# Performance work log

Hardware: AMD Instinct MI355X
Metric: run time of the kernel (lower is better)

## Reference

```python
import jax, jax.numpy as jnp
import numpy as np

X = Y = 512   # x_width = y_width
B = 8         # batch (<= bsize)
C = 32        # hidden_dim / num_feats
N_WARP = 3    # warp hidden layers
N_REND = 3    # renderer hidden layers
LRELU = 0.001


def _layer_norm(x, g, b, eps=1e-5):
    mu = x.mean(-1, keepdims=True)
    var = ((x - mu) ** 2).mean(-1, keepdims=True)
    return (x - mu) * jax.lax.rsqrt(var + eps) * g + b


def _grid_sample(img, grid):
    # img: (C,H,W) shared across batch; grid: (B,Hg,Wg,2) in [-1,1] (x,y)
    # bilinear, padding_mode='zeros', align_corners=False (torch defaults)
    Cc, H, W = img.shape
    ix = ((grid[..., 0] + 1.0) * W - 1.0) * 0.5
    iy = ((grid[..., 1] + 1.0) * H - 1.0) * 0.5
    x0f = jnp.floor(ix)
    y0f = jnp.floor(iy)
    wx1 = ix - x0f
    wy1 = iy - y0f

    def gather(xf, yf):
        valid = (xf >= 0) & (xf <= W - 1) & (yf >= 0) & (yf <= H - 1)
        xi = jnp.clip(xf, 0, W - 1).astype(jnp.int32)
        yi = jnp.clip(yf, 0, H - 1).astype(jnp.int32)
        v = img[:, yi, xi]                     # (C,B,Hg,Wg)
        return jnp.where(valid[None], v, 0.0)

    g00 = gather(x0f, y0f)
    g01 = gather(x0f + 1, y0f)
    g10 = gather(x0f, y0f + 1)
    g11 = gather(x0f + 1, y0f + 1)
    out = (g00 * ((1 - wx1) * (1 - wy1))[None]
           + g01 * (wx1 * (1 - wy1))[None]
           + g10 * ((1 - wx1) * wy1)[None]
           + g11 * (wx1 * wy1)[None])          # (C,B,Hg,Wg)
    return out.transpose(1, 0, 2, 3)           # (B,C,Hg,Wg)


def setup_inputs() -> dict:
    key = jax.random.key(0)
    ks = jax.random.split(key, 10)
    t = jax.random.uniform(ks[0], (B,), minval=-0.5, maxval=0.5)
    data = 0.1 * jax.random.normal(ks[1], (X, Y, C), dtype=jnp.float32)

    # G_FeatureTensor precomputed bilinear indices/weights (ds_factor=1)
    half = 0.5 / X
    xs = np.linspace(half, 1 - half, X, dtype=np.float64)
    xv, yv = np.meshgrid(xs, xs, indexing='ij')
    xy = np.stack([yv.ravel(), xv.ravel()], 1)          # (N,2) col0=yv col1=xv
    s = xy * np.array([X, Y], dtype=np.float64)
    idx = s.astype(np.int64)
    lerp_w = jnp.asarray(s - idx, dtype=jnp.float32)    # (N,2)
    x0 = jnp.asarray(np.clip(idx[:, 0], 0, X - 1), dtype=jnp.int32)
    y0 = jnp.asarray(np.clip(idx[:, 1], 0, Y - 1), dtype=jnp.int32)
    x1 = jnp.minimum(x0 + 1, X - 1)
    y1 = jnp.minimum(y0 + 1, Y - 1)

    lin = np.linspace(-1, 1, X, dtype=np.float32)
    gx, gy = np.meshgrid(lin, lin, indexing='xy')
    xy_basis = jnp.asarray(np.stack([gx, gy], -1))      # (X,Y,2)

    def lw(k, fan_in, shape):
        return (1.0 / np.sqrt(fan_in)) * jax.random.normal(k, shape, dtype=jnp.float32)

    kw = jax.random.split(ks[2], 8)
    return {
        't': t, 'data': data, 'lerp_w': lerp_w, 'xy_basis': xy_basis,
        'w_in': lw(kw[0], 3, (3, C)), 'b_in': jnp.zeros((C,)),
        'w_h': lw(kw[1], C, (N_WARP, C, C)), 'b_h': jnp.zeros((N_WARP, C)),
        'ln_g': jnp.ones((N_WARP, C)), 'ln_b': jnp.zeros((N_WARP, C)),
        'w_out': lw(kw[2], C, (C, 2)), 'b_out': jnp.zeros((2,)),
        'r_wh': lw(kw[3], C, (N_REND, C, C)), 'r_bh': jnp.zeros((N_REND, C)),
        'r_wo': lw(kw[4], C, (C, 1)), 'r_bo': jnp.zeros((1,)),
        'x0': x0, 'y0': y0, 'x1': x1, 'y1': y1,
    }


def reference(t, data, lerp_w, xy_basis, w_in, b_in, w_h, b_h, ln_g, ln_b,
              w_out, b_out, r_wh, r_bh, r_wo, r_bo, x0, y0, x1, y1):
    Bn = t.shape[0]
    wA = lerp_w[:, 0:1]
    wB = lerp_w[:, 1:2]
    # manual 4-corner bilinear gather over the learned feature grid
    feats = (data[y0, x0] * (1 - wA) * (1 - wB)
             + data[y0, x1] * wA * (1 - wB)
             + data[y1, x0] * (1 - wA) * wB
             + data[y1, x1] * wA * wB)                  # (N,C)
    feat_img = feats.reshape(X, Y, C).transpose(2, 0, 1)  # (C,X,Y)

    alpha = (t + 0.5)[:, None]                          # (B,1)
    t_emb = jnp.broadcast_to(alpha[:, None, None, :], (Bn, X, Y, 1))
    t_in = jnp.concatenate(
        [jnp.broadcast_to(xy_basis, (Bn, X, Y, 2)), t_emb], -1)  # (B,X,Y,3)

    h = t_in @ w_in + b_in
    for i in range(N_WARP):
        h = jnp.sin(_layer_norm(h @ w_h[i] + b_h[i], ln_g[i], ln_b[i]))
    motion = (h @ w_out + b_out) * 0.1                  # (B,X,Y,2)

    grid = motion + xy_basis                             # (B,X,Y,2)
    f = _grid_sample(feat_img, grid)                     # (B,C,X,Y)

    z = f.transpose(0, 2, 3, 1)
    for i in range(N_REND):
        z = jax.nn.relu(z @ r_wh[i] + r_bh[i])
    out = (z @ r_wo + r_bo).transpose(0, 3, 1, 2)        # (B,1,X,Y)
    return jnp.where(out >= 0, out, LRELU * out)
```

## Files before the change

### kernel.cpp

```cpp
#include <hip/hip_runtime.h>

#define XDIM 512
#define CDIM 32
#define NPIX (XDIM * XDIM)
#define NB 8

typedef short bf16x8 __attribute__((ext_vector_type(8)));
typedef float f32x4 __attribute__((ext_vector_type(4)));
typedef float f32x16 __attribute__((ext_vector_type(16)));

#define FEATS_BYTES (NPIX * CDIM * 4)

__device__ __forceinline__ short f2bf(float v) {
    __bf16 b = (__bf16)v;
    return __builtin_bit_cast(short, b);
}
__device__ __forceinline__ float bfup(short s) {
    return (float)__builtin_bit_cast(__bf16, s);
}

__global__ __launch_bounds__(64) void wprep_kernel(
    const float* __restrict__ w_h, const float* __restrict__ r_wh,
    unsigned short* __restrict__ afrag)
{
    int L = blockIdx.x >> 1;
    int T = blockIdx.x & 1;
    int l = threadIdx.x;
    const float* W = (L < 3) ? (w_h + L * CDIM * CDIM) : (r_wh + (L - 3) * CDIM * CDIM);
    int m = l & 31;
    int h = l >> 5;
    unsigned short* dh = afrag + (((L * 2 + T) * 2 + 0) * 64 + l) * 8;
    unsigned short* dl = afrag + (((L * 2 + T) * 2 + 1) * 64 + l) * 8;
    for (int j = 0; j < 8; j++) {
        int c = 16 * T + 4 * h + (j & 3) + 8 * (j >> 2);
        float v = W[c * CDIM + m];
        short hi = f2bf(v);
        short lo = f2bf(v - bfup(hi));
        dh[j] = (unsigned short)hi;
        dl[j] = (unsigned short)lo;
    }
}

__global__ __launch_bounds__(256) void feats_kernel(
    const float* __restrict__ data, const float* __restrict__ lerp_w,
    const int* __restrict__ x0, const int* __restrict__ y0,
    const int* __restrict__ x1, const int* __restrict__ y1,
    float* __restrict__ feats)
{
    int tid = blockIdx.x * 256 + threadIdx.x;
    int p = tid >> 5;
    int c = tid & 31;
    if (p >= NPIX) return;
    float wA = lerp_w[p * 2 + 0];
    float wB = lerp_w[p * 2 + 1];
    int xa = x0[p], ya = y0[p], xb = x1[p], yb = y1[p];
    float v00 = data[(ya * XDIM + xa) * CDIM + c];
    float v01 = data[(ya * XDIM + xb) * CDIM + c];
    float v10 = data[(yb * XDIM + xa) * CDIM + c];
    float v11 = data[(yb * XDIM + xb) * CDIM + c];
    float r = v00 * (1.f - wA) * (1.f - wB) + v01 * wA * (1.f - wB)
            + v10 * (1.f - wA) * wB + v11 * wA * wB;
    feats[p * CDIM + c] = r;
}

__device__ __forceinline__ void build2(const float a[16], bf16x8 bh[2], bf16x8 bl[2]) {
    #pragma unroll
    for (int r = 0; r < 16; r++) {
        short hi = f2bf(a[r]);
        bh[r >> 3][r & 7] = hi;
        bl[r >> 3][r & 7] = f2bf(a[r] - bfup(hi));
    }
}

__device__ __forceinline__ void matmul_split(
    const bf16x8 fh[2], const bf16x8 fl[2],
    const bf16x8 bh[2], const bf16x8 bl[2],
    f32x16& accA, f32x16& accB)
{
    f32x16 z = {0.f, 0.f, 0.f, 0.f, 0.f, 0.f, 0.f, 0.f,
                0.f, 0.f, 0.f, 0.f, 0.f, 0.f, 0.f, 0.f};
    accA = z; accB = z;
    accA = __builtin_amdgcn_mfma_f32_32x32x16_bf16(fl[0], bh[0], accA, 0, 0, 0);
    accB = __builtin_amdgcn_mfma_f32_32x32x16_bf16(fl[1], bh[1], accB, 0, 0, 0);
    accA = __builtin_amdgcn_mfma_f32_32x32x16_bf16(fh[0], bl[0], accA, 0, 0, 0);
    accB = __builtin_amdgcn_mfma_f32_32x32x16_bf16(fh[1], bl[1], accB, 0, 0, 0);
    accA = __builtin_amdgcn_mfma_f32_32x32x16_bf16(fh[0], bh[0], accA, 0, 0, 0);
    accB = __builtin_amdgcn_mfma_f32_32x32x16_bf16(fh[1], bh[1], accB, 0, 0, 0);
}

__device__ __forceinline__ void warp_layer(
    float a[16], const bf16x8 fh[2], const bf16x8 fl[2],
    const float* __restrict__ bias, const float* __restrict__ gamma,
    const float* __restrict__ beta, int h)
{
    bf16x8 bh[2], bl[2];
    build2(a, bh, bl);
    f32x16 accA, accB;
    matmul_split(fh, fl, bh, bl, accA, accB);

    float sum = 0.f, sq = 0.f;
    #pragma unroll
    for (int g = 0; g < 4; g++) {
        f32x4 bia = *(const f32x4*)(bias + 8 * g + 4 * h);
        #pragma unroll
        for (int i = 0; i < 4; i++) {
            int r = 4 * g + i;
            float v = (accA[r] + accB[r]) + bia[i];
            a[r] = v;
            sum += v;
            sq = fmaf(v, v, sq);
        }
    }
    sum += __shfl_xor(sum, 32, 64);
    sq  += __shfl_xor(sq, 32, 64);
    float mu = sum * (1.f / 32.f);
    float var = fmaf(sq, 1.f / 32.f, -mu * mu);
    float rs = rsqrtf(var + 1e-5f);
    #pragma unroll
    for (int g = 0; g < 4; g++) {
        f32x4 gg = *(const f32x4*)(gamma + 8 * g + 4 * h);
        f32x4 be = *(const f32x4*)(beta + 8 * g + 4 * h);
        #pragma unroll
        for (int i = 0; i < 4; i++) {
            int r = 4 * g + i;
            a[r] = __sinf(fmaf((a[r] - mu) * rs, gg[i], be[i]));
        }
    }
}

__device__ __forceinline__ void render_layer(
    float a[16], const bf16x8 fh[2], const bf16x8 fl[2],
    const float* __restrict__ bias, int h)
{
    bf16x8 bh[2], bl[2];
    build2(a, bh, bl);
    f32x16 accA, accB;
    matmul_split(fh, fl, bh, bl, accA, accB);
    #pragma unroll
    for (int g = 0; g < 4; g++) {
        f32x4 bia = *(const f32x4*)(bias + 8 * g + 4 * h);
        #pragma unroll
        for (int i = 0; i < 4; i++) {
            int r = 4 * g + i;
            a[r] = fmaxf((accA[r] + accB[r]) + bia[i], 0.f);
        }
    }
}

#define LOADFRAG(L, FH, FL) do { \
    FH[0] = ap[(((L) * 2 + 0) * 2 + 0) * 64 + lane]; \
    FL[0] = ap[(((L) * 2 + 0) * 2 + 1) * 64 + lane]; \
    FH[1] = ap[(((L) * 2 + 1) * 2 + 0) * 64 + lane]; \
    FL[1] = ap[(((L) * 2 + 1) * 2 + 1) * 64 + lane]; \
} while (0)

__global__ __launch_bounds__(256, 4) void fused_mfma_kernel(
    const float* __restrict__ t, const float* __restrict__ xy_basis,
    const float* __restrict__ w_in, const float* __restrict__ b_in,
    const float* __restrict__ b_h,
    const float* __restrict__ ln_g, const float* __restrict__ ln_b,
    const float* __restrict__ w_out, const float* __restrict__ b_out,
    const float* __restrict__ r_bh,
    const float* __restrict__ r_wo, const float* __restrict__ r_bo,
    const float* __restrict__ feats, const unsigned short* __restrict__ afrag,
    float* __restrict__ out)
{
    int lane = threadIdx.x & 63;
    int p = lane & 31, h = lane >> 5;

    int bid = blockIdx.x;
    int swz = (bid & 7) * 2048 + (bid >> 3);
    int gw = swz * 4 + (int)(threadIdx.x >> 6);
    int b = gw & 7;
    int pbase = (gw >> 3) << 5;
    int pix = pbase + p;

    const bf16x8* ap = (const bf16x8*)afrag;

    bf16x8 fAh[2], fAl[2], fBh[2], fBl[2], fCh[2], fCl[2];
    LOADFRAG(0, fAh, fAl);
    LOADFRAG(1, fBh, fBl);

    float alpha = t[b] + 0.5f;
    float2 xy = ((const float2*)xy_basis)[pix];

    float a[16];
    #pragma unroll
    for (int g = 0; g < 4; g++) {
        int c = 8 * g + 4 * h;
        f32x4 w0 = *(const f32x4*)(w_in + c);
        f32x4 w1 = *(const f32x4*)(w_in + CDIM + c);
        f32x4 w2 = *(const f32x4*)(w_in + 2 * CDIM + c);
        f32x4 bb = *(const f32x4*)(b_in + c);
        #pragma unroll
        for (int i = 0; i < 4; i++)
            a[4 * g + i] = fmaf(xy.x, w0[i], fmaf(xy.y, w1[i], fmaf(alpha, w2[i], bb[i])));
    }

    warp_layer(a, fAh, fAl, b_h + 0 * CDIM, ln_g + 0 * CDIM, ln_b + 0 * CDIM, h);
    LOADFRAG(2, fCh, fCl);
    warp_layer(a, fBh, fBl, b_h + 1 * CDIM, ln_g + 1 * CDIM, ln_b + 1 * CDIM, h);
    warp_layer(a, fCh, fCl, b_h + 2 * CDIM, ln_g + 2 * CDIM, ln_b + 2 * CDIM, h);

    float mx = 0.f, my = 0.f;
    #pragma unroll
    for (int g = 0; g < 4; g++) {
        int c = 8 * g + 4 * h;
        f32x4 wa = *(const f32x4*)(w_out + 2 * c);
        f32x4 wb = *(const f32x4*)(w_out + 2 * c + 4);
        mx = fmaf(a[4 * g + 0], wa[0], mx); my = fmaf(a[4 * g + 0], wa[1], my);
        mx = fmaf(a[4 * g + 1], wa[2], mx); my = fmaf(a[4 * g + 1], wa[3], my);
        mx = fmaf(a[4 * g + 2], wb[0], mx); my = fmaf(a[4 * g + 2], wb[1], my);
        mx = fmaf(a[4 * g + 3], wb[2], mx); my = fmaf(a[4 * g + 3], wb[3], my);
    }
    mx += __shfl_xor(mx, 32, 64);
    my += __shfl_xor(my, 32, 64);
    float gridx = fmaf(mx + b_out[0], 0.1f, xy.x);
    float gridy = fmaf(my + b_out[1], 0.1f, xy.y);

    bf16x8 r0h[2], r0l[2], r1h[2], r1l[2], r2h[2], r2l[2];
    LOADFRAG(3, r0h, r0l);
    LOADFRAG(4, r1h, r1l);
    LOADFRAG(5, r2h, r2l);

    float ix = ((gridx + 1.0f) * (float)XDIM - 1.0f) * 0.5f;
    float iy = ((gridy + 1.0f) * (float)XDIM - 1.0f) * 0.5f;
    float x0f = floorf(ix), y0f = floorf(iy);
    float wx = ix - x0f, wy = iy - y0f;
    #pragma unroll
    for (int r = 0; r < 16; r++) a[r] = 0.f;
    #pragma unroll
    for (int corner = 0; corner < 4; corner++) {
        float xf = x0f + (float)(corner & 1);
        float yf = y0f + (float)(corner >> 1);
        float w = ((corner & 1) ? wx : 1.f - wx) * ((corner >> 1) ? wy : 1.f - wy);
        bool valid = (xf >= 0.f) && (xf <= (float)(XDIM - 1)) &&
                     (yf >= 0.f) && (yf <= (float)(XDIM - 1));
        if (!valid) w = 0.f;
        int xi = (int)fminf(fmaxf(xf, 0.f), (float)(XDIM - 1));
        int yi = (int)fminf(fmaxf(yf, 0.f), (float)(XDIM - 1));
        const float* fp = feats + (yi * XDIM + xi) * CDIM + 4 * h;
        #pragma unroll
        for (int g = 0; g < 4; g++) {
            f32x4 v = *(const f32x4*)(fp + 8 * g);
            #pragma unroll
            for (int i = 0; i < 4; i++)
                a[4 * g + i] = fmaf(w, v[i], a[4 * g + i]);
        }
    }

    render_layer(a, r0h, r0l, r_bh + 0 * CDIM, h);
    render_layer(a, r1h, r1l, r_bh + 1 * CDIM, h);
    render_layer(a, r2h, r2l, r_bh + 2 * CDIM, h);

    float o = 0.f;
    #pragma unroll
    for (int g = 0; g < 4; g++) {
        f32x4 wz = *(const f32x4*)(r_wo + 8 * g + 4 * h);
        #pragma unroll
        for (int i = 0; i < 4; i++) o = fmaf(a[4 * g + i], wz[i], o);
    }
    o += __shfl_xor(o, 32, 64);
    o += r_bo[0];
    o = (o >= 0.f) ? o : 0.001f * o;
    if (h == 0) out[b * NPIX + pix] = o;
}

extern "C" void kernel_launch(void* const* d_in, const int* in_sizes, int n_in,
                              void* d_out, int out_size, void* d_ws, size_t ws_size,
                              hipStream_t stream) {
    const float* t        = (const float*)d_in[0];
    const float* data     = (const float*)d_in[1];
    const float* lerp_w   = (const float*)d_in[2];
    const float* xy_basis = (const float*)d_in[3];
    const float* w_in     = (const float*)d_in[4];
    const float* b_in     = (const float*)d_in[5];
    const float* w_h      = (const float*)d_in[6];
    const float* b_h      = (const float*)d_in[7];
    const float* ln_g     = (const float*)d_in[8];
    const float* ln_b     = (const float*)d_in[9];
    const float* w_out    = (const float*)d_in[10];
    const float* b_out    = (const float*)d_in[11];
    const float* r_wh     = (const float*)d_in[12];
    const float* r_bh     = (const float*)d_in[13];
    const float* r_wo     = (const float*)d_in[14];
    const float* r_bo     = (const float*)d_in[15];
    const int* x0 = (const int*)d_in[16];
    const int* y0 = (const int*)d_in[17];
    const int* x1 = (const int*)d_in[18];
    const int* y1 = (const int*)d_in[19];

    float* feats = (float*)d_ws;
    unsigned short* afrag = (unsigned short*)((char*)d_ws + FEATS_BYTES);
    float* out = (float*)d_out;

    wprep_kernel<<<12, 64, 0, stream>>>(w_h, r_wh, afrag);
    feats_kernel<<<(NPIX * CDIM) / 256, 256, 0, stream>>>(data, lerp_w, x0, y0, x1, y1, feats);
    fused_mfma_kernel<<<(NB * NPIX) / 128, 256, 0, stream>>>(
        t, xy_basis, w_in, b_in, b_h, ln_g, ln_b, w_out, b_out,
        r_bh, r_wo, r_bo, feats, afrag, out);
}
```

Baseline: 321.0 us.

## Split fused kernel into separate warp-MLP and render kernels via grid buffer

Splits the single fused per-pixel kernel into two launches: one computes the warp MLP and writes sampling coordinates to a workspace buffer, the other reads them, does the bilinear feature gather and runs the renderer MLP. The aim is lower register pressure and better latency hiding for the gather in each kernel, since each only holds its own weight fragments. The cost is an extra launch and a round trip of 16 MB of grid data through global memory. It falls back to the fused kernel if the workspace is too small.

Result: slower. 328.5 us (+2.3%).

```diff
diff --git a/kernel.cpp b/kernel.cpp
--- a/kernel.cpp
+++ b/kernel.cpp
@@ -10,6 +10,9 @@
 typedef float f32x16 __attribute__((ext_vector_type(16)));
 
 #define FEATS_BYTES (NPIX * CDIM * 4)
+#define AFRAG_BYTES 32768
+#define GRID_BYTES (NB * NPIX * 8)
+#define WS_NEED (FEATS_BYTES + AFRAG_BYTES + GRID_BYTES)
 
 __device__ __forceinline__ short f2bf(float v) {
     __bf16 b = (__bf16)v;
@@ -154,6 +157,131 @@
     FL[1] = ap[(((L) * 2 + 1) * 2 + 1) * 64 + lane]; \
 } while (0)
 
+#define PIXMAP() \
+    int lane = threadIdx.x & 63; \
+    int p = lane & 31, h = lane >> 5; \
+    int bid = blockIdx.x; \
+    int swz = (bid & 7) * 2048 + (bid >> 3); \
+    int gw = swz * 4 + (int)(threadIdx.x >> 6); \
+    int b = gw & 7; \
+    int pbase = (gw >> 3) << 5; \
+    int pix = pbase + p;
+
+__global__ __launch_bounds__(256, 4) void warp_kernel(
+    const float* __restrict__ t, const float* __restrict__ xy_basis,
+    const float* __restrict__ w_in, const float* __restrict__ b_in,
+    const float* __restrict__ b_h,
+    const float* __restrict__ ln_g, const float* __restrict__ ln_b,
+    const float* __restrict__ w_out, const float* __restrict__ b_out,
+    const unsigned short* __restrict__ afrag, float2* __restrict__ grid)
+{
+    PIXMAP();
+    const bf16x8* ap = (const bf16x8*)afrag;
+
+    bf16x8 fAh[2], fAl[2], fBh[2], fBl[2], fCh[2], fCl[2];
+    LOADFRAG(0, fAh, fAl);
+    LOADFRAG(1, fBh, fBl);
+
+    float alpha = t[b] + 0.5f;
+    float2 xy = ((const float2*)xy_basis)[pix];
+
+    float a[16];
+    #pragma unroll
+    for (int g = 0; g < 4; g++) {
+        int c = 8 * g + 4 * h;
+        f32x4 w0 = *(const f32x4*)(w_in + c);
+        f32x4 w1 = *(const f32x4*)(w_in + CDIM + c);
+        f32x4 w2 = *(const f32x4*)(w_in + 2 * CDIM + c);
+        f32x4 bb = *(const f32x4*)(b_in + c);
+        #pragma unroll
+        for (int i = 0; i < 4; i++)
+            a[4 * g + i] = fmaf(xy.x, w0[i], fmaf(xy.y, w1[i], fmaf(alpha, w2[i], bb[i])));
+    }
+
+    warp_layer(a, fAh, fAl, b_h + 0 * CDIM, ln_g + 0 * CDIM, ln_b + 0 * CDIM, h);
+    LOADFRAG(2, fCh, fCl);
+    warp_layer(a, fBh, fBl, b_h + 1 * CDIM, ln_g + 1 * CDIM, ln_b + 1 * CDIM, h);
+    warp_layer(a, fCh, fCl, b_h + 2 * CDIM, ln_g + 2 * CDIM, ln_b + 2 * CDIM, h);
+
+    float mx = 0.f, my = 0.f;
+    #pragma unroll
+    for (int g = 0; g < 4; g++) {
+        int c = 8 * g + 4 * h;
+        f32x4 wa = *(const f32x4*)(w_out + 2 * c);
+        f32x4 wb = *(const f32x4*)(w_out + 2 * c + 4);
+        mx = fmaf(a[4 * g + 0], wa[0], mx); my = fmaf(a[4 * g + 0], wa[1], my);
+        mx = fmaf(a[4 * g + 1], wa[2], mx); my = fmaf(a[4 * g + 1], wa[3], my);
+        mx = fmaf(a[4 * g + 2], wb[0], mx); my = fmaf(a[4 * g + 2], wb[1], my);
+        mx = fmaf(a[4 * g + 3], wb[2], mx); my = fmaf(a[4 * g + 3], wb[3], my);
+    }
+    mx += __shfl_xor(mx, 32, 64);
+    my += __shfl_xor(my, 32, 64);
+    float gridx = fmaf(mx + b_out[0], 0.1f, xy.x);
+    float gridy = fmaf(my + b_out[1], 0.1f, xy.y);
+    if (h == 0) grid[b * NPIX + pix] = make_float2(gridx, gridy);
+}
+
+__global__ __launch_bounds__(256, 4) void render_kernel(
+    const float2* __restrict__ grid,
+    const float* __restrict__ r_bh,
+    const float* __restrict__ r_wo, const float* __restrict__ r_bo,
+    const float* __restrict__ feats, const unsigned short* __restrict__ afrag,
+    float* __restrict__ out)
+{
+    PIXMAP();
+    const bf16x8* ap = (const bf16x8*)afrag;
+
+    bf16x8 r0h[2], r0l[2], r1h[2], r1l[2], r2h[2], r2l[2];
+    LOADFRAG(3, r0h, r0l);
+    LOADFRAG(4, r1h, r1l);
+    LOADFRAG(5, r2h, r2l);
+
+    float2 gxy = grid[b * NPIX + pix];
+
+    float ix = ((gxy.x + 1.0f) * (float)XDIM - 1.0f) * 0.5f;
+    float iy = ((gxy.y + 1.0f) * (float)XDIM - 1.0f) * 0.5f;
+    float x0f = floorf(ix), y0f = floorf(iy);
+    float wx = ix - x0f, wy = iy - y0f;
+    float a[16];
+    #pragma unroll
+    for (int r = 0; r < 16; r++) a[r] = 0.f;
+    #pragma unroll
+    for (int corner = 0; corner < 4; corner++) {
+        float xf = x0f + (float)(corner & 1);
+        float yf = y0f + (float)(corner >> 1);
+        float w = ((corner & 1) ? wx : 1.f - wx) * ((corner >> 1) ? wy : 1.f - wy);
+        bool valid = (xf >= 0.f) && (xf <= (float)(XDIM - 1)) &&
+                     (yf >= 0.f) && (yf <= (float)(XDIM - 1));
+        if (!valid) w = 0.f;
+        int xi = (int)fminf(fmaxf(xf, 0.f), (float)(XDIM - 1));
+        int yi = (int)fminf(fmaxf(yf, 0.f), (float)(XDIM - 1));
+        const float* fp = feats + (yi * XDIM + xi) * CDIM + 4 * h;
+        #pragma unroll
+        for (int g = 0; g < 4; g++) {
+            f32x4 v = *(const f32x4*)(fp + 8 * g);
+            #pragma unroll
+            for (int i = 0; i < 4; i++)
+                a[4 * g + i] = fmaf(w, v[i], a[4 * g + i]);
+        }
+    }
+
+    render_layer(a, r0h, r0l, r_bh + 0 * CDIM, h);
+    render_layer(a, r1h, r1l, r_bh + 1 * CDIM, h);
+    render_layer(a, r2h, r2l, r_bh + 2 * CDIM, h);
+
+    float o = 0.f;
+    #pragma unroll
+    for (int g = 0; g < 4; g++) {
+        f32x4 wz = *(const f32x4*)(r_wo + 8 * g + 4 * h);
+        #pragma unroll
+        for (int i = 0; i < 4; i++) o = fmaf(a[4 * g + i], wz[i], o);
+    }
+    o += __shfl_xor(o, 32, 64);
+    o += r_bo[0];
+    o = (o >= 0.f) ? o : 0.001f * o;
+    if (h == 0) out[b * NPIX + pix] = o;
+}
+
 __global__ __launch_bounds__(256, 4) void fused_mfma_kernel(
     const float* __restrict__ t, const float* __restrict__ xy_basis,
     const float* __restrict__ w_in, const float* __restrict__ b_in,
@@ -165,16 +293,7 @@
     const float* __restrict__ feats, const unsigned short* __restrict__ afrag,
     float* __restrict__ out)
 {
-    int lane = threadIdx.x & 63;
-    int p = lane & 31, h = lane >> 5;
-
-    int bid = blockIdx.x;
-    int swz = (bid & 7) * 2048 + (bid >> 3);
-    int gw = swz * 4 + (int)(threadIdx.x >> 6);
-    int b = gw & 7;
-    int pbase = (gw >> 3) << 5;
-    int pix = pbase + p;
-
+    PIXMAP();
     const bf16x8* ap = (const bf16x8*)afrag;
 
     bf16x8 fAh[2], fAl[2], fBh[2], fBl[2], fCh[2], fCl[2];
@@ -292,11 +411,20 @@
 
     float* feats = (float*)d_ws;
     unsigned short* afrag = (unsigned short*)((char*)d_ws + FEATS_BYTES);
+    float2* grid = (float2*)((char*)d_ws + FEATS_BYTES + AFRAG_BYTES);
     float* out = (float*)d_out;
 
     wprep_kernel<<<12, 64, 0, stream>>>(w_h, r_wh, afrag);
     feats_kernel<<<(NPIX * CDIM) / 256, 256, 0, stream>>>(data, lerp_w, x0, y0, x1, y1, feats);
-    fused_mfma_kernel<<<(NB * NPIX) / 128, 256, 0, stream>>>(
-        t, xy_basis, w_in, b_in, b_h, ln_g, ln_b, w_out, b_out,
-        r_bh, r_wo, r_bo, feats, afrag, out);
-}
+
+    if (ws_size >= (size_t)WS_NEED) {
+        warp_kernel<<<(NB * NPIX) / 128, 256, 0, stream>>>(
+            t, xy_basis, w_in, b_in, b_h, ln_g, ln_b, w_out, b_out, afrag, grid);
+        render_kernel<<<(NB * NPIX) / 128, 256, 0, stream>>>(
+            grid, r_bh, r_wo, r_bo, feats, afrag, out);
+    } else {
+        fused_mfma_kernel<<<(NB * NPIX) / 128, 256, 0, stream>>>(
+            t, xy_basis, w_in, b_in, b_h, ln_g, ln_b, w_out, b_out,
+            r_bh, r_wo, r_bo, feats, afrag, out);
+    }
+}
```

## Fold first renderer layer into feature grid before grid sampling

Applied to the files above, without the earlier changes.

Bilinear grid sampling is linear, so the first renderer matmul is now applied once per grid pixel in a new y_kernel, rather than once per batch item after sampling. The fused kernel samples the pre-multiplied features and then only adds the bias and ReLU for that layer, skipping its MFMA work across all eight batch items. This adds an extra pass over the 32 MB feature buffer, done in place, which is safe only because each pixel's 32 channels sit in one wavefront. It also wraps the MFMA sequence in s_setprio to raise wave priority during matrix ops.

After: 644.1 us. 2.01x slower.

```diff
diff --git a/kernel.cpp b/kernel.cpp
--- a/kernel.cpp
+++ b/kernel.cpp
@@ -63,6 +63,20 @@
     feats[p * CDIM + c] = r;
 }
 
+__global__ __launch_bounds__(256) void y_kernel(
+    const float* __restrict__ r_wh, float* __restrict__ feats)
+{
+    int tid = blockIdx.x * 256 + threadIdx.x;
+    int p = tid >> 5;
+    int c = tid & 31;
+    const float* f = feats + p * CDIM;
+    float acc = 0.f;
+    #pragma unroll
+    for (int k = 0; k < CDIM; k++)
+        acc = fmaf(f[k], r_wh[k * CDIM + c], acc);
+    feats[p * CDIM + c] = acc;
+}
+
 __device__ __forceinline__ void build2(const float a[16], bf16x8 bh[2], bf16x8 bl[2]) {
     #pragma unroll
     for (int r = 0; r < 16; r++) {
@@ -80,12 +94,14 @@
     f32x16 z = {0.f, 0.f, 0.f, 0.f, 0.f, 0.f, 0.f, 0.f,
                 0.f, 0.f, 0.f, 0.f, 0.f, 0.f, 0.f, 0.f};
     accA = z; accB = z;
+    __builtin_amdgcn_s_setprio(1);
     accA = __builtin_amdgcn_mfma_f32_32x32x16_bf16(fl[0], bh[0], accA, 0, 0, 0);
     accB = __builtin_amdgcn_mfma_f32_32x32x16_bf16(fl[1], bh[1], accB, 0, 0, 0);
     accA = __builtin_amdgcn_mfma_f32_32x32x16_bf16(fh[0], bl[0], accA, 0, 0, 0);
     accB = __builtin_amdgcn_mfma_f32_32x32x16_bf16(fh[1], bl[1], accB, 0, 0, 0);
     accA = __builtin_amdgcn_mfma_f32_32x32x16_bf16(fh[0], bh[0], accA, 0, 0, 0);
     accB = __builtin_amdgcn_mfma_f32_32x32x16_bf16(fh[1], bh[1], accB, 0, 0, 0);
+    __builtin_amdgcn_s_setprio(0);
 }
 
 __device__ __forceinline__ void warp_layer(
@@ -162,7 +178,7 @@
     const float* __restrict__ w_out, const float* __restrict__ b_out,
     const float* __restrict__ r_bh,
     const float* __restrict__ r_wo, const float* __restrict__ r_bo,
-    const float* __restrict__ feats, const unsigned short* __restrict__ afrag,
+    const float* __restrict__ yimg, const unsigned short* __restrict__ afrag,
     float* __restrict__ out)
 {
     int lane = threadIdx.x & 63;
@@ -218,8 +234,7 @@
     float gridx = fmaf(mx + b_out[0], 0.1f, xy.x);
     float gridy = fmaf(my + b_out[1], 0.1f, xy.y);
 
-    bf16x8 r0h[2], r0l[2], r1h[2], r1l[2], r2h[2], r2l[2];
-    LOADFRAG(3, r0h, r0l);
+    bf16x8 r1h[2], r1l[2], r2h[2], r2l[2];
     LOADFRAG(4, r1h, r1l);
     LOADFRAG(5, r2h, r2l);
 
@@ -239,7 +254,7 @@
         if (!valid) w = 0.f;
         int xi = (int)fminf(fmaxf(xf, 0.f), (float)(XDIM - 1));
         int yi = (int)fminf(fmaxf(yf, 0.f), (float)(XDIM - 1));
-        const float* fp = feats + (yi * XDIM + xi) * CDIM + 4 * h;
+        const float* fp = yimg + (yi * XDIM + xi) * CDIM + 4 * h;
         #pragma unroll
         for (int g = 0; g < 4; g++) {
             f32x4 v = *(const f32x4*)(fp + 8 * g);
@@ -248,8 +263,14 @@
                 a[4 * g + i] = fmaf(w, v[i], a[4 * g + i]);
         }
     }
-
-    render_layer(a, r0h, r0l, r_bh + 0 * CDIM, h);
+    #pragma unroll
+    for (int g = 0; g < 4; g++) {
+        f32x4 bia = *(const f32x4*)(r_bh + 0 * CDIM + 8 * g + 4 * h);
+        #pragma unroll
+        for (int i = 0; i < 4; i++)
+            a[4 * g + i] = fmaxf(a[4 * g + i] + bia[i], 0.f);
+    }
+
     render_layer(a, r1h, r1l, r_bh + 1 * CDIM, h);
     render_layer(a, r2h, r2l, r_bh + 2 * CDIM, h);
 
@@ -296,6 +317,7 @@
 
     wprep_kernel<<<12, 64, 0, stream>>>(w_h, r_wh, afrag);
     feats_kernel<<<(NPIX * CDIM) / 256, 256, 0, stream>>>(data, lerp_w, x0, y0, x1, y1, feats);
+    y_kernel<<<(NPIX * CDIM) / 256, 256, 0, stream>>>(r_wh, feats);
     fused_mfma_kernel<<<(NB * NPIX) / 128, 256, 0, stream>>>(
         t, xy_basis, w_in, b_in, b_h, ln_g, ln_b, w_out, b_out,
         r_bh, r_wo, r_bo, feats, afrag, out);
```

## Process two batch items per wavefront to reuse weight fragments and add ILP

Applied to the files above, without the earlier changes.

Each wavefront now handles the same 32 pixels for two batch indices (b and b+4), interleaving the warp MLP, gather and render layers for both. Weight fragments and bias loads are shared across the two items, the grid halves, and the independent MFMA chains can overlap. The cost is roughly double the live accumulator registers, and the occupancy hint of 4 blocks per SM was dropped from launch bounds, so occupancy may fall.

New measurement: 270.1 us. -15.9%, faster.

```diff
diff --git a/kernel.cpp b/kernel.cpp
--- a/kernel.cpp
+++ b/kernel.cpp
@@ -147,61 +147,10 @@
     }
 }
 
-#define LOADFRAG(L, FH, FL) do { \
-    FH[0] = ap[(((L) * 2 + 0) * 2 + 0) * 64 + lane]; \
-    FL[0] = ap[(((L) * 2 + 0) * 2 + 1) * 64 + lane]; \
-    FH[1] = ap[(((L) * 2 + 1) * 2 + 0) * 64 + lane]; \
-    FL[1] = ap[(((L) * 2 + 1) * 2 + 1) * 64 + lane]; \
-} while (0)
-
-__global__ __launch_bounds__(256, 4) void fused_mfma_kernel(
-    const float* __restrict__ t, const float* __restrict__ xy_basis,
-    const float* __restrict__ w_in, const float* __restrict__ b_in,
-    const float* __restrict__ b_h,
-    const float* __restrict__ ln_g, const float* __restrict__ ln_b,
-    const float* __restrict__ w_out, const float* __restrict__ b_out,
-    const float* __restrict__ r_bh,
-    const float* __restrict__ r_wo, const float* __restrict__ r_bo,
-    const float* __restrict__ feats, const unsigned short* __restrict__ afrag,
-    float* __restrict__ out)
-{
-    int lane = threadIdx.x & 63;
-    int p = lane & 31, h = lane >> 5;
-
-    int bid = blockIdx.x;
-    int swz = (bid & 7) * 2048 + (bid >> 3);
-    int gw = swz * 4 + (int)(threadIdx.x >> 6);
-    int b = gw & 7;
-    int pbase = (gw >> 3) << 5;
-    int pix = pbase + p;
-
-    const bf16x8* ap = (const bf16x8*)afrag;
-
-    bf16x8 fAh[2], fAl[2], fBh[2], fBl[2], fCh[2], fCl[2];
-    LOADFRAG(0, fAh, fAl);
-    LOADFRAG(1, fBh, fBl);
-
-    float alpha = t[b] + 0.5f;
-    float2 xy = ((const float2*)xy_basis)[pix];
-
-    float a[16];
-    #pragma unroll
-    for (int g = 0; g < 4; g++) {
-        int c = 8 * g + 4 * h;
-        f32x4 w0 = *(const f32x4*)(w_in + c);
-        f32x4 w1 = *(const f32x4*)(w_in + CDIM + c);
-        f32x4 w2 = *(const f32x4*)(w_in + 2 * CDIM + c);
-        f32x4 bb = *(const f32x4*)(b_in + c);
-        #pragma unroll
-        for (int i = 0; i < 4; i++)
-            a[4 * g + i] = fmaf(xy.x, w0[i], fmaf(xy.y, w1[i], fmaf(alpha, w2[i], bb[i])));
-    }
-
-    warp_layer(a, fAh, fAl, b_h + 0 * CDIM, ln_g + 0 * CDIM, ln_b + 0 * CDIM, h);
-    LOADFRAG(2, fCh, fCl);
-    warp_layer(a, fBh, fBl, b_h + 1 * CDIM, ln_g + 1 * CDIM, ln_b + 1 * CDIM, h);
-    warp_layer(a, fCh, fCl, b_h + 2 * CDIM, ln_g + 2 * CDIM, ln_b + 2 * CDIM, h);
-
+__device__ __forceinline__ void motion_head(
+    const float a[16], const float* __restrict__ w_out, int h,
+    float& mxo, float& myo)
+{
     float mx = 0.f, my = 0.f;
     #pragma unroll
     for (int g = 0; g < 4; g++) {
@@ -215,14 +164,13 @@
     }
     mx += __shfl_xor(mx, 32, 64);
     my += __shfl_xor(my, 32, 64);
-    float gridx = fmaf(mx + b_out[0], 0.1f, xy.x);
-    float gridy = fmaf(my + b_out[1], 0.1f, xy.y);
-
-    bf16x8 r0h[2], r0l[2], r1h[2], r1l[2], r2h[2], r2l[2];
-    LOADFRAG(3, r0h, r0l);
-    LOADFRAG(4, r1h, r1l);
-    LOADFRAG(5, r2h, r2l);
-
+    mxo = mx; myo = my;
+}
+
+__device__ __forceinline__ void do_gather(
+    float a[16], float gridx, float gridy,
+    const float* __restrict__ feats, int h)
+{
     float ix = ((gridx + 1.0f) * (float)XDIM - 1.0f) * 0.5f;
     float iy = ((gridy + 1.0f) * (float)XDIM - 1.0f) * 0.5f;
     float x0f = floorf(ix), y0f = floorf(iy);
@@ -248,11 +196,11 @@
                 a[4 * g + i] = fmaf(w, v[i], a[4 * g + i]);
         }
     }
-
-    render_layer(a, r0h, r0l, r_bh + 0 * CDIM, h);
-    render_layer(a, r1h, r1l, r_bh + 1 * CDIM, h);
-    render_layer(a, r2h, r2l, r_bh + 2 * CDIM, h);
-
+}
+
+__device__ __forceinline__ float out_head(
+    const float a[16], const float* __restrict__ r_wo, int h)
+{
     float o = 0.f;
     #pragma unroll
     for (int g = 0; g < 4; g++) {
@@ -261,9 +209,105 @@
         for (int i = 0; i < 4; i++) o = fmaf(a[4 * g + i], wz[i], o);
     }
     o += __shfl_xor(o, 32, 64);
-    o += r_bo[0];
-    o = (o >= 0.f) ? o : 0.001f * o;
-    if (h == 0) out[b * NPIX + pix] = o;
+    return o;
+}
+
+#define LOADFRAG(L, FH, FL) do { \
+    FH[0] = ap[(((L) * 2 + 0) * 2 + 0) * 64 + lane]; \
+    FL[0] = ap[(((L) * 2 + 0) * 2 + 1) * 64 + lane]; \
+    FH[1] = ap[(((L) * 2 + 1) * 2 + 0) * 64 + lane]; \
+    FL[1] = ap[(((L) * 2 + 1) * 2 + 1) * 64 + lane]; \
+} while (0)
+
+__global__ __launch_bounds__(256) void fused_mfma_kernel(
+    const float* __restrict__ t, const float* __restrict__ xy_basis,
+    const float* __restrict__ w_in, const float* __restrict__ b_in,
+    const float* __restrict__ b_h,
+    const float* __restrict__ ln_g, const float* __restrict__ ln_b,
+    const float* __restrict__ w_out, const float* __restrict__ b_out,
+    const float* __restrict__ r_bh,
+    const float* __restrict__ r_wo, const float* __restrict__ r_bo,
+    const float* __restrict__ feats, const unsigned short* __restrict__ afrag,
+    float* __restrict__ out)
+{
+    int lane = threadIdx.x & 63;
+    int p = lane & 31, h = lane >> 5;
+
+    int bid = blockIdx.x;
+    int swz = (bid & 7) * 1024 + (bid >> 3);
+    int gw = swz * 4 + (int)(threadIdx.x >> 6);
+    int bp = gw & 3;
+    int b0 = bp, b1 = bp + 4;
+    int pbase = (gw >> 2) << 5;
+    int pix = pbase + p;
+
+    const bf16x8* ap = (const bf16x8*)afrag;
+
+    bf16x8 fAh[2], fAl[2], fBh[2], fBl[2], fCh[2], fCl[2];
+    LOADFRAG(0, fAh, fAl);
+    LOADFRAG(1, fBh, fBl);
+
+    float alpha0 = t[b0] + 0.5f;
+    float alpha1 = t[b1] + 0.5f;
+    float2 xy = ((const float2*)xy_basis)[pix];
+
+    float a0[16], a1[16];
+    #pragma unroll
+    for (int g = 0; g < 4; g++) {
+        int c = 8 * g + 4 * h;
+        f32x4 w0 = *(const f32x4*)(w_in + c);
+        f32x4 w1 = *(const f32x4*)(w_in + CDIM + c);
+        f32x4 w2 = *(const f32x4*)(w_in + 2 * CDIM + c);
+        f32x4 bb = *(const f32x4*)(b_in + c);
+        #pragma unroll
+        for (int i = 0; i < 4; i++) {
+            a0[4 * g + i] = fmaf(xy.x, w0[i], fmaf(xy.y, w1[i], fmaf(alpha0, w2[i], bb[i])));
+            a1[4 * g + i] = fmaf(xy.x, w0[i], fmaf(xy.y, w1[i], fmaf(alpha1, w2[i], bb[i])));
+        }
+    }
+
+    warp_layer(a0, fAh, fAl, b_h + 0 * CDIM, ln_g + 0 * CDIM, ln_b + 0 * CDIM, h);
+    warp_layer(a1, fAh, fAl, b_h + 0 * CDIM, ln_g + 0 * CDIM, ln_b + 0 * CDIM, h);
+    LOADFRAG(2, fCh, fCl);
+    warp_layer(a0, fBh, fBl, b_h + 1 * CDIM, ln_g + 1 * CDIM, ln_b + 1 * CDIM, h);
+    warp_layer(a1, fBh, fBl, b_h + 1 * CDIM, ln_g + 1 * CDIM, ln_b + 1 * CDIM, h);
+    warp_layer(a0, fCh, fCl, b_h + 2 * CDIM, ln_g + 2 * CDIM, ln_b + 2 * CDIM, h);
+    warp_layer(a1, fCh, fCl, b_h + 2 * CDIM, ln_g + 2 * CDIM, ln_b + 2 * CDIM, h);
+
+    float mx0, my0, mx1, my1;
+    motion_head(a0, w_out, h, mx0, my0);
+    motion_head(a1, w_out, h, mx1, my1);
+    float bo0 = b_out[0], bo1 = b_out[1];
+    float gx0 = fmaf(mx0 + bo0, 0.1f, xy.x);
+    float gy0 = fmaf(my0 + bo1, 0.1f, xy.y);
+    float gx1 = fmaf(mx1 + bo0, 0.1f, xy.x);
+    float gy1 = fmaf(my1 + bo1, 0.1f, xy.y);
+
+    bf16x8 r0h[2], r0l[2], r1h[2], r1l[2], r2h[2], r2l[2];
+    LOADFRAG(3, r0h, r0l);
+    LOADFRAG(4, r1h, r1l);
+    LOADFRAG(5, r2h, r2l);
+
+    do_gather(a0, gx0, gy0, feats, h);
+    do_gather(a1, gx1, gy1, feats, h);
+
+    render_layer(a0, r0h, r0l, r_bh + 0 * CDIM, h);
+    render_layer(a1, r0h, r0l, r_bh + 0 * CDIM, h);
+    render_layer(a0, r1h, r1l, r_bh + 1 * CDIM, h);
+    render_layer(a1, r1h, r1l, r_bh + 1 * CDIM, h);
+    render_layer(a0, r2h, r2l, r_bh + 2 * CDIM, h);
+    render_layer(a1, r2h, r2l, r_bh + 2 * CDIM, h);
+
+    float o0 = out_head(a0, r_wo, h);
+    float o1 = out_head(a1, r_wo, h);
+    float rbo = r_bo[0];
+    o0 += rbo; o1 += rbo;
+    o0 = (o0 >= 0.f) ? o0 : 0.001f * o0;
+    o1 = (o1 >= 0.f) ? o1 : 0.001f * o1;
+    if (h == 0) {
+        out[b0 * NPIX + pix] = o0;
+        out[b1 * NPIX + pix] = o1;
+    }
 }
 
 extern "C" void kernel_launch(void* const* d_in, const int* in_sizes, int n_in,
@@ -296,7 +340,7 @@
 
     wprep_kernel<<<12, 64, 0, stream>>>(w_h, r_wh, afrag);
     feats_kernel<<<(NPIX * CDIM) / 256, 256, 0, stream>>>(data, lerp_w, x0, y0, x1, y1, feats);
-    fused_mfma_kernel<<<(NB * NPIX) / 128, 256, 0, stream>>>(
+    fused_mfma_kernel<<<(NB * NPIX) / 256, 256, 0, stream>>>(
         t, xy_basis, w_in, b_in, b_h, ln_g, ln_b, w_out, b_out,
         r_bh, r_wo, r_bo, feats, afrag, out);
 }
```
